# Performance work log

Measured on AMD Instinct MI355X. Metric: run time of the kernel, lower is better.

Reference implementation:

```python
import jax, jax.numpy as jnp
import numpy as np

D = 1024          # model_dim
BD = D // 2       # bottleneck_dim
K = 64            # num_splats
B, S = 8, 2048


def setup_inputs() -> dict:
    key = jax.random.key(0)
    ks = jax.random.split(key, 12)
    sc = 0.02
    return {
        "token_embeddings": jax.random.normal(ks[0], (B, S, D), jnp.float32),
        "splat_influences": jax.random.uniform(ks[1], (B, S, K), jnp.float32),
        # encoder: Linear(D -> BD), stored [in, out]
        "enc_W": jax.random.normal(ks[2], (D, BD), jnp.float32) * sc,
        "enc_b": jnp.zeros((BD,), jnp.float32),
        # per-splat transforms: K x Linear(BD -> BD)
        "trans_W": jax.random.normal(ks[3], (K, BD, BD), jnp.float32) * sc,
        "trans_b": jnp.zeros((K, BD), jnp.float32),
        # decoder: Linear(BD -> D)
        "dec_W": jax.random.normal(ks[4], (BD, D), jnp.float32) * sc,
        "dec_b": jnp.zeros((D,), jnp.float32),
        # flow gate: Linear(D -> D) + sigmoid
        "gate_W": jax.random.normal(ks[5], (D, D), jnp.float32) * sc,
        "gate_b": jnp.zeros((D,), jnp.float32),
    }


def reference(token_embeddings, splat_influences, enc_W, enc_b,
              trans_W, trans_b, dec_W, dec_b, gate_W, gate_b):
    # gather: [B,K,S] @ [B,S,D] -> [B,K,D]
    influences_t = jnp.swapaxes(splat_influences, 1, 2)          # [B,K,S]
    gathered = jnp.einsum('bks,bsd->bkd', influences_t, token_embeddings)
    total = jnp.clip(influences_t.sum(axis=2, keepdims=True), 1e-8, None)  # [B,K,1]
    gathered = gathered / total
    # encoder (dropout inactive at eval)
    encoded = jax.nn.relu(gathered @ enc_W + enc_b)              # [B,K,BD]
    # per-splat transform as grouped matmul
    transformed = jnp.einsum('bkd,kde->bke', encoded, trans_W) + trans_b  # [B,K,BD]
    decoded = transformed @ dec_W + dec_b                        # [B,K,D]
    # scatter back to tokens: [B,S,K] @ [B,K,D]
    flow = jnp.einsum('bsk,bkd->bsd', splat_influences, decoded)
    gate = jax.nn.sigmoid(token_embeddings @ gate_W + gate_b)    # [B,S,D]
    return flow * gate
```

## Files before the change

### kernel.cpp

```cpp
#include <hip/hip_runtime.h>

#define BB 8
#define SS 2048
#define DD 1024
#define BDD 512
#define NSP 64

typedef __attribute__((ext_vector_type(8))) short bf16x8;
typedef __attribute__((ext_vector_type(4))) float f32x4;
typedef unsigned short u16;
typedef unsigned int u32;

__device__ __forceinline__ u16 f2bf(float f) {
  u32 u = __builtin_bit_cast(u32, f);
  u = u + 0x7fffu + ((u >> 16) & 1u);
  return (u16)(u >> 16);
}

__device__ __forceinline__ void gl_lds16(const void* g, void* l) {
  __builtin_amdgcn_global_load_lds((const __attribute__((address_space(1))) void*)g,
                                   (__attribute__((address_space(3))) void*)l,
                                   16, 0, 0);
}

__global__ void k_prep_tok(const float* __restrict__ tok, u16* __restrict__ tokbf,
                           u16* __restrict__ tokT) {
  __shared__ u16 tile[64][80];
  int C0 = blockIdx.x * 64;
  int R0 = blockIdx.y * 64;
  int b = R0 >> 11, s0 = R0 & 2047;
  int t = threadIdx.x;
  int lr = t >> 3, lc = (t & 7) * 8;
#pragma unroll
  for (int i = 0; i < 2; ++i) {
    int r = lr + i * 32;
    const float* src = tok + (size_t)(R0 + r) * DD + C0 + lc;
    float4 a = *(const float4*)src;
    float4 bq = *(const float4*)(src + 4);
    uint4 v;
    v.x = f2bf(a.x) | ((u32)f2bf(a.y) << 16);
    v.y = f2bf(a.z) | ((u32)f2bf(a.w) << 16);
    v.z = f2bf(bq.x) | ((u32)f2bf(bq.y) << 16);
    v.w = f2bf(bq.z) | ((u32)f2bf(bq.w) << 16);
    *(uint4*)(tokbf + (size_t)(R0 + r) * DD + C0 + lc) = v;
    *(uint4*)&tile[r][lc] = v;
  }
  __syncthreads();
  int sseg = (t & 7) * 8;
#pragma unroll
  for (int i = 0; i < 2; ++i) {
    int dcol = (t >> 3) + i * 32;
    u16 a0 = tile[sseg + 0][dcol], a1 = tile[sseg + 1][dcol];
    u16 a2 = tile[sseg + 2][dcol], a3 = tile[sseg + 3][dcol];
    u16 a4 = tile[sseg + 4][dcol], a5 = tile[sseg + 5][dcol];
    u16 a6 = tile[sseg + 6][dcol], a7 = tile[sseg + 7][dcol];
    uint4 v;
    v.x = a0 | ((u32)a1 << 16);
    v.y = a2 | ((u32)a3 << 16);
    v.z = a4 | ((u32)a5 << 16);
    v.w = a6 | ((u32)a7 << 16);
    *(uint4*)(tokT + (size_t)b * DD * SS + (size_t)(C0 + dcol) * SS + s0 + sseg) = v;
  }
}

__global__ void k_prep_infl(const float* __restrict__ infl, u16* __restrict__ inflbf,
                            u16* __restrict__ inflT, float* __restrict__ rsum) {
  __shared__ u16 tile[64][80];
  __shared__ float ps[32][64];
  int R0 = blockIdx.x * 64;
  int b = R0 >> 11, s0 = R0 & 2047;
  int st = s0 >> 6;
  int t = threadIdx.x;
  int lr = t >> 3, lc = (t & 7) * 8;
  float col[8];
#pragma unroll
  for (int j = 0; j < 8; ++j) col[j] = 0.f;
#pragma unroll
  for (int i = 0; i < 2; ++i) {
    int r = lr + i * 32;
    const float* src = infl + (size_t)(R0 + r) * NSP + lc;
    float4 a = *(const float4*)src;
    float4 bq = *(const float4*)(src + 4);
    col[0] += a.x; col[1] += a.y; col[2] += a.z; col[3] += a.w;
    col[4] += bq.x; col[5] += bq.y; col[6] += bq.z; col[7] += bq.w;
    uint4 v;
    v.x = f2bf(a.x) | ((u32)f2bf(a.y) << 16);
    v.y = f2bf(a.z) | ((u32)f2bf(a.w) << 16);
    v.z = f2bf(bq.x) | ((u32)f2bf(bq.y) << 16);
    v.w = f2bf(bq.z) | ((u32)f2bf(bq.w) << 16);
    *(uint4*)(inflbf + (size_t)(R0 + r) * NSP + lc) = v;
    *(uint4*)&tile[r][lc] = v;
  }
#pragma unroll
  for (int j = 0; j < 8; ++j) ps[lr][lc + j] = col[j];
  __syncthreads();
  if (t < 64) {
    float s = 0.f;
#pragma unroll
    for (int rr = 0; rr < 32; ++rr) s += ps[rr][t];
    rsum[((size_t)b * 32 + st) * 64 + t] = s;
  }
  int sseg = (t & 7) * 8;
#pragma unroll
  for (int i = 0; i < 2; ++i) {
    int dcol = (t >> 3) + i * 32;
    u16 a0 = tile[sseg + 0][dcol], a1 = tile[sseg + 1][dcol];
    u16 a2 = tile[sseg + 2][dcol], a3 = tile[sseg + 3][dcol];
    u16 a4 = tile[sseg + 4][dcol], a5 = tile[sseg + 5][dcol];
    u16 a6 = tile[sseg + 6][dcol], a7 = tile[sseg + 7][dcol];
    uint4 v;
    v.x = a0 | ((u32)a1 << 16);
    v.y = a2 | ((u32)a3 << 16);
    v.z = a4 | ((u32)a5 << 16);
    v.w = a6 | ((u32)a7 << 16);
    *(uint4*)(inflT + ((size_t)b * NSP + dcol) * SS + s0 + sseg) = v;
  }
}

__global__ void k_tot_fin(const float* __restrict__ rsum, float* __restrict__ rtot) {
  int t = threadIdx.x;
  float s = 0.f;
#pragma unroll
  for (int st = 0; st < 32; ++st)
    s += rsum[((size_t)(t >> 6) * 32 + st) * 64 + (t & 63)];
  rtot[t] = 1.f / fmaxf(s, 1e-8f);
}

__global__ void k_gatewt(const float* __restrict__ gw, u16* __restrict__ gwt) {
  __shared__ float tile[32][33];
  int n0 = blockIdx.x * 32, k0 = blockIdx.y * 32;
  int tx = threadIdx.x & 31, ty = threadIdx.x >> 5;
#pragma unroll
  for (int r = 0; r < 4; ++r) {
    int kr = ty + r * 8;
    tile[kr][tx] = gw[(k0 + kr) * DD + n0 + tx];
  }
  __syncthreads();
#pragma unroll
  for (int r = 0; r < 4; ++r) {
    int nc = ty + r * 8;
    gwt[(n0 + nc) * DD + k0 + tx] = f2bf(tile[tx][nc]);
  }
}

__global__ __launch_bounds__(256) void k_gather_mfma(const u16* __restrict__ inflT,
                                                     const u16* __restrict__ tokT,
                                                     float* __restrict__ pg) {
  __shared__ u16 As[64 * 64];
  __shared__ u16 Bs[64 * 64];
  int t = threadIdx.x;
  int l = t & 63, w = t >> 6;
  int wr = w >> 1, wc = w & 1;
  int n0 = blockIdx.x * 64;
  int b = blockIdx.y;
  int sq = blockIdx.z;
  int l15 = l & 15, lh = l >> 4;
  int srow = t >> 3, scol = (t & 7) * 8;

  const u16* ap = inflT + (size_t)b * NSP * SS;
  const u16* bp = tokT + (size_t)b * DD * SS;

  f32x4 acc[2][2];
#pragma unroll
  for (int i = 0; i < 2; ++i)
#pragma unroll
    for (int j = 0; j < 2; ++j) acc[i][j] = (f32x4){0.f, 0.f, 0.f, 0.f};

  for (int kt = 0; kt < 8; ++kt) {
    int k0 = sq * 512 + kt * 64;
#pragma unroll
    for (int i = 0; i < 2; ++i) {
      int row = srow + i * 32;
      gl_lds16(ap + row * SS + k0 + scol, &As[row * 64 + scol]);
      gl_lds16(bp + (n0 + row) * SS + k0 + scol, &Bs[row * 64 + scol]);
    }
    __syncthreads();
#pragma unroll
    for (int ks = 0; ks < 2; ++ks) {
      bf16x8 af[2], bfv[2];
#pragma unroll
      for (int mi = 0; mi < 2; ++mi)
        af[mi] = *(const bf16x8*)&As[(wr * 32 + mi * 16 + l15) * 64 + ks * 32 + lh * 8];
#pragma unroll
      for (int ni = 0; ni < 2; ++ni)
        bfv[ni] = *(const bf16x8*)&Bs[(wc * 32 + ni * 16 + l15) * 64 + ks * 32 + lh * 8];
#pragma unroll
      for (int mi = 0; mi < 2; ++mi)
#pragma unroll
        for (int ni = 0; ni < 2; ++ni)
          acc[mi][ni] = __builtin_amdgcn_mfma_f32_16x16x32_bf16(af[mi], bfv[ni], acc[mi][ni], 0, 0, 0);
    }
    __syncthreads();
  }

#pragma unroll
  for (int mi = 0; mi < 2; ++mi)
#pragma unroll
    for (int ni = 0; ni < 2; ++ni)
#pragma unroll
      for (int r = 0; r < 4; ++r) {
        int krow = wr * 32 + mi * 16 + lh * 4 + r;
        int dcol = n0 + wc * 32 + ni * 16 + l15;
        pg[((size_t)sq * 512 + b * NSP + krow) * DD + dcol] = acc[mi][ni][r];
      }
}

__global__ void k_enc_part(const float* __restrict__ pg, const float* __restrict__ rtot,
                           const float* __restrict__ encW, float* __restrict__ pe) {
  __shared__ float gl[8][64];
  int dq = blockIdx.x, mt = blockIdx.y;
  int m0 = mt * 8, d0 = dq * 64;
  int t = threadIdx.x;
  {
    int r = t >> 5, c = t & 31;
    float s1 = 0.f, s2 = 0.f;
#pragma unroll
    for (int q = 0; q < 4; ++q) {
      const float* qp = pg + ((size_t)q * 512 + m0 + r) * DD + d0;
      s1 += qp[c]; s2 += qp[c + 32];
    }
    float rt = rtot[m0 + r];
    gl[r][c] = s1 * rt;
    gl[r][c + 32] = s2 * rt;
  }
  __syncthreads();
  int n4 = (t & 127) * 4, mh = (t >> 7) * 4;
  float4 acc[4];
#pragma unroll
  for (int m = 0; m < 4; ++m) acc[m] = (float4){0.f, 0.f, 0.f, 0.f};
  for (int i = 0; i < 64; ++i) {
    float4 wv = *(const float4*)(encW + (d0 + i) * BDD + n4);
#pragma unroll
    for (int m = 0; m < 4; ++m) {
      float g = gl[mh + m][i];
      acc[m].x += g * wv.x; acc[m].y += g * wv.y;
      acc[m].z += g * wv.z; acc[m].w += g * wv.w;
    }
  }
#pragma unroll
  for (int m = 0; m < 4; ++m)
    *(float4*)(pe + ((size_t)dq * 512 + m0 + mh + m) * BDD + n4) = acc[m];
}

__global__ void k_trans_part(const float* __restrict__ pe, const float* __restrict__ encB,
                             const float* __restrict__ trW, float* __restrict__ pt) {
  __shared__ float el[8][32];
  int dq = blockIdx.x, ks = blockIdx.y;
  int d0 = dq * 32;
  int t = threadIdx.x;
  {
    int r = t >> 5, c = t & 31;
    int m = r * NSP + ks;
    float s = 0.f;
#pragma unroll
    for (int p = 0; p < 16; ++p)
      s += pe[((size_t)p * 512 + m) * BDD + d0 + c];
    el[r][c] = fmaxf(s + encB[d0 + c], 0.f);
  }
  __syncthreads();
  int n4 = (t & 127) * 4, mh = (t >> 7) * 4;
  float4 acc[4];
#pragma unroll
  for (int m = 0; m < 4; ++m) acc[m] = (float4){0.f, 0.f, 0.f, 0.f};
  for (int i = 0; i < 32; ++i) {
    float4 wv = *(const float4*)(trW + ((size_t)ks * BDD + d0 + i) * BDD + n4);
#pragma unroll
    for (int m = 0; m < 4; ++m) {
      float g = el[mh + m][i];
      acc[m].x += g * wv.x; acc[m].y += g * wv.y;
      acc[m].z += g * wv.z; acc[m].w += g * wv.w;
    }
  }
#pragma unroll
  for (int m = 0; m < 4; ++m)
    *(float4*)(pt + ((size_t)dq * 512 + (mh + m) * NSP + ks) * BDD + n4) = acc[m];
}

__global__ void k_dec_part(const float* __restrict__ pt, const float* __restrict__ trB,
                           const float* __restrict__ decW, float* __restrict__ pd) {
  __shared__ float tl[8][64];
  int dq = blockIdx.x, mt = blockIdx.y;
  int m0 = mt * 8, d0 = dq * 64;
  int t = threadIdx.x;
  {
    int r = t >> 5, c = t & 31;
    int m = m0 + r;
    float s1 = 0.f, s2 = 0.f;
#pragma unroll
    for (int p = 0; p < 16; ++p) {
      const float* qp = pt + ((size_t)p * 512 + m) * BDD + d0;
      s1 += qp[c]; s2 += qp[c + 32];
    }
    tl[r][c] = s1 + trB[(m & 63) * BDD + d0 + c];
    tl[r][c + 32] = s2 + trB[(m & 63) * BDD + d0 + c + 32];
  }
  __syncthreads();
  int n4 = t * 4;
  float4 acc[8];
#pragma unroll
  for (int m = 0; m < 8; ++m) acc[m] = (float4){0.f, 0.f, 0.f, 0.f};
  for (int i = 0; i < 64; ++i) {
    float4 wv = *(const float4*)(decW + (d0 + i) * DD + n4);
#pragma unroll
    for (int m = 0; m < 8; ++m) {
      float g = tl[m][i];
      acc[m].x += g * wv.x; acc[m].y += g * wv.y;
      acc[m].z += g * wv.z; acc[m].w += g * wv.w;
    }
  }
#pragma unroll
  for (int m = 0; m < 8; ++m)
    *(float4*)(pd + ((size_t)dq * 512 + m0 + m) * DD + n4) = acc[m];
}

__global__ void red_dec(const float* __restrict__ pd, const float* __restrict__ decB,
                        u16* __restrict__ decT) {
  __shared__ u16 st[64][34];
  int nt = blockIdx.x, b = blockIdx.y;
  int n0 = nt * 32;
  int t = threadIdx.x;
  int nn = t & 31, kg = t >> 5;
  float db = decB[n0 + nn];
#pragma unroll
  for (int ki = 0; ki < 8; ++ki) {
    int ks = kg * 8 + ki;
    float s = db;
#pragma unroll
    for (int p = 0; p < 8; ++p)
      s += pd[((size_t)p * 512 + b * NSP + ks) * DD + n0 + nn];
    st[ks][nn] = f2bf(s);
  }
  __syncthreads();
  int nr = t >> 3, kseg = (t & 7) * 8;
  uint4 v;
  v.x = st[kseg + 0][nr] | ((u32)st[kseg + 1][nr] << 16);
  v.y = st[kseg + 2][nr] | ((u32)st[kseg + 3][nr] << 16);
  v.z = st[kseg + 4][nr] | ((u32)st[kseg + 5][nr] << 16);
  v.w = st[kseg + 6][nr] | ((u32)st[kseg + 7][nr] << 16);
  *(uint4*)(decT + ((size_t)b * DD + n0 + nr) * NSP + kseg) = v;
}

__global__ __launch_bounds__(512) void k_out(const u16* __restrict__ tokbf,
                                             const u16* __restrict__ gwt,
                                             const u16* __restrict__ inflbf,
                                             const u16* __restrict__ decT,
                                             const float* __restrict__ gateB,
                                             float* __restrict__ outp) {
  __shared__ u16 As[3][128 * 64];
  __shared__ u16 Bs[3][256 * 64];
  int t = threadIdx.x;
  int l = t & 63, w = t >> 6;
  int wr = w >> 2, wc = w & 3;
  int m0 = blockIdx.x * 128, n0 = blockIdx.y * 256;
  int l15 = l & 15, lh = l >> 4;

  auto stage = [&](int sl, int kt) {
    int k0 = kt * 64;
#pragma unroll
    for (int p = 0; p < 2; ++p) {
      int e = p * 512 + t;
      int row = e >> 3, csrc = ((e & 7) ^ (row & 7)) * 8;
      gl_lds16(tokbf + (size_t)(m0 + row) * DD + k0 + csrc, &As[sl][e * 8]);
    }
#pragma unroll
    for (int p = 0; p < 4; ++p) {
      int e = p * 512 + t;
      int row = e >> 3, csrc = ((e & 7) ^ (row & 7)) * 8;
      gl_lds16(gwt + (size_t)(n0 + row) * DD + k0 + csrc, &Bs[sl][e * 8]);
    }
  };

  auto compute = [&](int sl, f32x4 (&acc)[4][4]) {
#pragma unroll
    for (int ks = 0; ks < 2; ++ks) {
      bf16x8 af[4], bfv[4];
      int g = ks * 4 + lh;
#pragma unroll
      for (int mi = 0; mi < 4; ++mi) {
        int r = wr * 64 + mi * 16 + l15;
        af[mi] = *(const bf16x8*)&As[sl][r * 64 + (g ^ (r & 7)) * 8];
      }
#pragma unroll
      for (int ni = 0; ni < 4; ++ni) {
        int r = wc * 64 + ni * 16 + l15;
        bfv[ni] = *(const bf16x8*)&Bs[sl][r * 64 + (g ^ (r & 7)) * 8];
      }
      __builtin_amdgcn_s_setprio(1);
#pragma unroll
      for (int mi = 0; mi < 4; ++mi)
#pragma unroll
        for (int ni = 0; ni < 4; ++ni)
          acc[mi][ni] = __builtin_amdgcn_mfma_f32_16x16x32_bf16(af[mi], bfv[ni], acc[mi][ni], 0, 0, 0);
      __builtin_amdgcn_s_setprio(0);
    }
  };

  f32x4 accg[4][4];
#pragma unroll
  for (int i = 0; i < 4; ++i)
#pragma unroll
    for (int j = 0; j < 4; ++j) accg[i][j] = (f32x4){0.f, 0.f, 0.f, 0.f};

  stage(0, 0);
  stage(1, 1);

  for (int kt = 0; kt < 14; ++kt) {
    stage((kt + 2) % 3, kt + 2);
    asm volatile("s_waitcnt vmcnt(12)" ::: "memory");
    __builtin_amdgcn_s_barrier();
    compute(kt % 3, accg);
    __builtin_amdgcn_s_barrier();
  }
  asm volatile("s_waitcnt vmcnt(6)" ::: "memory");
  __builtin_amdgcn_s_barrier();
  compute(2, accg);
  __builtin_amdgcn_s_barrier();
  asm volatile("s_waitcnt vmcnt(0)" ::: "memory");
  __builtin_amdgcn_s_barrier();
  compute(0, accg);
  __builtin_amdgcn_s_barrier();

  int b = m0 >> 11;
  int s0m = m0 & 2047;
#pragma unroll
  for (int p = 0; p < 2; ++p) {
    int e = p * 512 + t;
    int row = e >> 3, csrc = ((e & 7) ^ (row & 7)) * 8;
    gl_lds16(inflbf + ((size_t)b * SS + s0m + row) * NSP + csrc, &As[0][e * 8]);
  }
#pragma unroll
  for (int p = 0; p < 4; ++p) {
    int e = p * 512 + t;
    int row = e >> 3, csrc = ((e & 7) ^ (row & 7)) * 8;
    gl_lds16(decT + ((size_t)b * DD + n0 + row) * NSP + csrc, &Bs[0][e * 8]);
  }
  asm volatile("s_waitcnt vmcnt(0)" ::: "memory");
  __builtin_amdgcn_s_barrier();

  f32x4 accf[4][4];
#pragma unroll
  for (int i = 0; i < 4; ++i)
#pragma unroll
    for (int j = 0; j < 4; ++j) accf[i][j] = (f32x4){0.f, 0.f, 0.f, 0.f};
  compute(0, accf);

  float gb[4];
#pragma unroll
  for (int ni = 0; ni < 4; ++ni) gb[ni] = gateB[n0 + wc * 64 + ni * 16 + l15];
#pragma unroll
  for (int mi = 0; mi < 4; ++mi)
#pragma unroll
    for (int ni = 0; ni < 4; ++ni)
#pragma unroll
      for (int r = 0; r < 4; ++r) {
        int mr = m0 + wr * 64 + mi * 16 + lh * 4 + r;
        int nc = n0 + wc * 64 + ni * 16 + l15;
        float z = accg[mi][ni][r] + gb[ni];
        float gate = 1.f / (1.f + __expf(-z));
        outp[(size_t)mr * DD + nc] = accf[mi][ni][r] * gate;
      }
}

extern "C" void kernel_launch(void* const* d_in, const int* in_sizes, int n_in,
                              void* d_out, int out_size, void* d_ws, size_t ws_size,
                              hipStream_t stream) {
  const float* tok = (const float*)d_in[0];
  const float* infl = (const float*)d_in[1];
  const float* encW = (const float*)d_in[2];
  const float* encB = (const float*)d_in[3];
  const float* trW = (const float*)d_in[4];
  const float* trB = (const float*)d_in[5];
  const float* decW = (const float*)d_in[6];
  const float* decB = (const float*)d_in[7];
  const float* gw = (const float*)d_in[8];
  const float* gateB = (const float*)d_in[9];
  float* outp = (float*)d_out;

  char* wsp = (char*)d_ws;
  u16* tokbf = (u16*)(wsp);
  u16* gwt = (u16*)(wsp + 33554432);
  u16* inflbf = (u16*)(wsp + 35651584);
  float* rtot = (float*)(wsp + 37748736);
  u16* decT = (u16*)(wsp + 41945088);
  u16* tokT = (u16*)(wsp + 42993664);
  float* pe = (float*)(wsp + 42993664);
  float* pt = (float*)(wsp + 42993664 + 16777216);
  u16* inflT = (u16*)(wsp + 76548096);
  float* rsum = (float*)(wsp + 78645248);
  float* scratch = (float*)(wsp + 78710784);

  k_prep_tok<<<dim3(16, 256), dim3(256), 0, stream>>>(tok, tokbf, tokT);
  k_prep_infl<<<dim3(256), dim3(256), 0, stream>>>(infl, inflbf, inflT, rsum);
  k_tot_fin<<<dim3(1), dim3(512), 0, stream>>>(rsum, rtot);
  k_gatewt<<<dim3(32, 32), dim3(256), 0, stream>>>(gw, gwt);
  k_gather_mfma<<<dim3(16, 8, 4), dim3(256), 0, stream>>>(inflT, tokT, scratch);
  k_enc_part<<<dim3(16, 64), dim3(256), 0, stream>>>(scratch, rtot, encW, pe);
  k_trans_part<<<dim3(16, 64), dim3(256), 0, stream>>>(pe, encB, trW, pt);
  k_dec_part<<<dim3(8, 64), dim3(256), 0, stream>>>(pt, trB, decW, scratch);
  red_dec<<<dim3(32, 8), dim3(256), 0, stream>>>(scratch, decB, decT);
  k_out<<<dim3(128, 4), dim3(512), 0, stream>>>(tokbf, gwt, inflbf, decT, gateB, outp);
}
```

Before: 180.5 us.

## Switch k_out gate GEMM to double-buffered LDS with loads interleaved into MFMA phases

Replaces the three-slot LDS pipeline in the output kernel with a two-slot ping-pong. The next tile's global-to-LDS loads are issued inside each MFMA half-phase, after the fragment reads, so memory traffic overlaps compute at a finer grain. This cuts LDS use by a third and adds a launch-bounds hint asking for two blocks per CU. The intent is more latency hiding and possibly higher occupancy. In exchange, prefetch depth drops to one tile with a full vmcnt(0) wait each half-iteration, and the tighter register budget may cause spills.

```diff
diff --git a/kernel.cpp b/kernel.cpp
--- a/kernel.cpp
+++ b/kernel.cpp
@@ -340,85 +340,81 @@
   *(uint4*)(decT + ((size_t)b * DD + n0 + nr) * NSP + kseg) = v;
 }
 
-__global__ __launch_bounds__(512) void k_out(const u16* __restrict__ tokbf,
-                                             const u16* __restrict__ gwt,
-                                             const u16* __restrict__ inflbf,
-                                             const u16* __restrict__ decT,
-                                             const float* __restrict__ gateB,
-                                             float* __restrict__ outp) {
-  __shared__ u16 As[3][128 * 64];
-  __shared__ u16 Bs[3][256 * 64];
+
+#define STAGE_A(sl, k0, p)                                                  \
+  { int e = (p)*512 + t; int row = e >> 3, csrc = ((e & 7) ^ (row & 7)) * 8; \
+    gl_lds16(tokbf + (size_t)(m0 + row) * DD + (k0) + csrc, &As[sl][e * 8]); }
+#define STAGE_B(sl, k0, p)                                                  \
+  { int e = (p)*512 + t; int row = e >> 3, csrc = ((e & 7) ^ (row & 7)) * 8; \
+    gl_lds16(gwt + (size_t)(n0 + row) * DD + (k0) + csrc, &Bs[sl][e * 8]); }
+
+#define PHASE(sl, ks, ACC, STAGE_STMT)                                       \
+  {                                                                          \
+    bf16x8 af[4], bfv[4];                                                    \
+    int g = (ks)*4 + lh;                                                     \
+    _Pragma("unroll")                                                        \
+    for (int mi = 0; mi < 4; ++mi) {                                         \
+      int r = wr * 64 + mi * 16 + l15;                                       \
+      af[mi] = *(const bf16x8*)&As[sl][r * 64 + (g ^ (r & 7)) * 8];          \
+    }                                                                        \
+    _Pragma("unroll")                                                        \
+    for (int ni = 0; ni < 4; ++ni) {                                         \
+      int r = wc * 64 + ni * 16 + l15;                                       \
+      bfv[ni] = *(const bf16x8*)&Bs[sl][r * 64 + (g ^ (r & 7)) * 8];         \
+    }                                                                        \
+    STAGE_STMT;                                                              \
+    __builtin_amdgcn_s_setprio(1);                                           \
+    _Pragma("unroll")                                                        \
+    for (int mi = 0; mi < 4; ++mi)                                           \
+      _Pragma("unroll")                                                      \
+      for (int ni = 0; ni < 4; ++ni)                                         \
+        ACC[mi][ni] = __builtin_amdgcn_mfma_f32_16x16x32_bf16(af[mi], bfv[ni], ACC[mi][ni], 0, 0, 0); \
+    __builtin_amdgcn_s_setprio(0);                                           \
+  }
+
+__global__ __launch_bounds__(512, 2) void k_out(const u16* __restrict__ tokbf,
+                                                const u16* __restrict__ gwt,
+                                                const u16* __restrict__ inflbf,
+                                                const u16* __restrict__ decT,
+                                                const float* __restrict__ gateB,
+                                                float* __restrict__ outp) {
+  __shared__ u16 As[2][128 * 64];
+  __shared__ u16 Bs[2][256 * 64];
   int t = threadIdx.x;
   int l = t & 63, w = t >> 6;
   int wr = w >> 2, wc = w & 3;
   int m0 = blockIdx.x * 128, n0 = blockIdx.y * 256;
   int l15 = l & 15, lh = l >> 4;
 
-  auto stage = [&](int sl, int kt) {
-    int k0 = kt * 64;
-#pragma unroll
-    for (int p = 0; p < 2; ++p) {
-      int e = p * 512 + t;
-      int row = e >> 3, csrc = ((e & 7) ^ (row & 7)) * 8;
-      gl_lds16(tokbf + (size_t)(m0 + row) * DD + k0 + csrc, &As[sl][e * 8]);
-    }
-#pragma unroll
-    for (int p = 0; p < 4; ++p) {
-      int e = p * 512 + t;
-      int row = e >> 3, csrc = ((e & 7) ^ (row & 7)) * 8;
-      gl_lds16(gwt + (size_t)(n0 + row) * DD + k0 + csrc, &Bs[sl][e * 8]);
-    }
-  };
-
-  auto compute = [&](int sl, f32x4 (&acc)[4][4]) {
-#pragma unroll
-    for (int ks = 0; ks < 2; ++ks) {
-      bf16x8 af[4], bfv[4];
-      int g = ks * 4 + lh;
-#pragma unroll
-      for (int mi = 0; mi < 4; ++mi) {
-        int r = wr * 64 + mi * 16 + l15;
-        af[mi] = *(const bf16x8*)&As[sl][r * 64 + (g ^ (r & 7)) * 8];
-      }
-#pragma unroll
-      for (int ni = 0; ni < 4; ++ni) {
-        int r = wc * 64 + ni * 16 + l15;
-        bfv[ni] = *(const bf16x8*)&Bs[sl][r * 64 + (g ^ (r & 7)) * 8];
-      }
-      __builtin_amdgcn_s_setprio(1);
-#pragma unroll
-      for (int mi = 0; mi < 4; ++mi)
-#pragma unroll
-        for (int ni = 0; ni < 4; ++ni)
-          acc[mi][ni] = __builtin_amdgcn_mfma_f32_16x16x32_bf16(af[mi], bfv[ni], acc[mi][ni], 0, 0, 0);
-      __builtin_amdgcn_s_setprio(0);
-    }
-  };
-
   f32x4 accg[4][4];
 #pragma unroll
   for (int i = 0; i < 4; ++i)
 #pragma unroll
     for (int j = 0; j < 4; ++j) accg[i][j] = (f32x4){0.f, 0.f, 0.f, 0.f};
 
-  stage(0, 0);
-  stage(1, 1);
-
-  for (int kt = 0; kt < 14; ++kt) {
-    stage((kt + 2) % 3, kt + 2);
-    asm volatile("s_waitcnt vmcnt(12)" ::: "memory");
-    __builtin_amdgcn_s_barrier();
-    compute(kt % 3, accg);
-    __builtin_amdgcn_s_barrier();
-  }
-  asm volatile("s_waitcnt vmcnt(6)" ::: "memory");
-  __builtin_amdgcn_s_barrier();
-  compute(2, accg);
-  __builtin_amdgcn_s_barrier();
+  STAGE_A(0, 0, 0); STAGE_B(0, 0, 0); STAGE_B(0, 0, 1);
+  STAGE_A(0, 0, 1); STAGE_B(0, 0, 2); STAGE_B(0, 0, 3);
   asm volatile("s_waitcnt vmcnt(0)" ::: "memory");
   __builtin_amdgcn_s_barrier();
-  compute(0, accg);
-  __builtin_amdgcn_s_barrier();
+
+#pragma unroll 1
+  for (int i = 0; i < 8; ++i) {
+    int kb = i * 128 + 64;
+    int kc = kb + 64;
+    PHASE(0, 0, accg, { STAGE_A(1, kb, 0); STAGE_B(1, kb, 0); STAGE_B(1, kb, 1); });
+    PHASE(0, 1, accg, { STAGE_A(1, kb, 1); STAGE_B(1, kb, 2); STAGE_B(1, kb, 3); });
+    asm volatile("s_waitcnt vmcnt(0)" ::: "memory");
+    __builtin_amdgcn_s_barrier();
+    if (i < 7) {
+      PHASE(1, 0, accg, { STAGE_A(0, kc, 0); STAGE_B(0, kc, 0); STAGE_B(0, kc, 1); });
+      PHASE(1, 1, accg, { STAGE_A(0, kc, 1); STAGE_B(0, kc, 2); STAGE_B(0, kc, 3); });
+    } else {
+      PHASE(1, 0, accg, {});
+      PHASE(1, 1, accg, {});
+    }
+    asm volatile("s_waitcnt vmcnt(0)" ::: "memory");
+    __builtin_amdgcn_s_barrier();
+  }
 
   int b = m0 >> 11;
   int s0m = m0 & 2047;
@@ -442,7 +438,8 @@
   for (int i = 0; i < 4; ++i)
 #pragma unroll
     for (int j = 0; j < 4; ++j) accf[i][j] = (f32x4){0.f, 0.f, 0.f, 0.f};
-  compute(0, accf);
+  PHASE(0, 0, accf, {});
+  PHASE(0, 1, accf, {});
 
   float gb[4];
 #pragma unroll
```

New measurement: 173.4 us. 1.04x faster.
